# Kernel optimization log

Measured on AMD Instinct MI355X. Metric: run time of the kernel, lower is better.

## Reference

```python
import jax, jax.numpy as jnp
import numpy as np

MARGIN = 0.5
EPS = 1e-5
NOISE_RATE = 0.5


def setup_inputs() -> dict:
    key = jax.random.key(0)
    k1, k2, k3, k4, k5 = jax.random.split(key, 5)
    n, m, d, c = 1024, 65536, 512, 10000
    return {
        "inputs_col": jax.random.normal(k1, (n, d), dtype=jnp.float32),
        "inputs_row": jax.random.normal(k2, (m, d), dtype=jnp.float32),
        "center": jax.random.normal(k3, (c, d), dtype=jnp.float32),
        "targets_col": jax.random.randint(k4, (n,), 0, c, dtype=jnp.int64),
        "target_row": jax.random.randint(k5, (m,), 0, c, dtype=jnp.int64),
        "filled_mask": jnp.ones((c,), dtype=bool),
    }


def _prism_keep(features, targets, center, filled_mask, noise_rate):
    # no_grad in the original -> stop_gradient here
    f = jax.lax.stop_gradient(features)
    c = jax.lax.stop_gradient(center)
    # all_sim_exp[cls] / sum(all_sim_exp) is exactly softmax over class logits
    probs = jax.nn.softmax(f @ c.T, axis=-1)          # [n, num_classes]
    sel = jnp.take_along_axis(probs, targets[:, None], axis=1)[:, 0]  # [n]
    C = jnp.where(filled_mask[targets], sel, 1.0)      # not-in-memory -> 1
    n = C.shape[0]
    n_remove = int(noise_rate * n)                     # static
    to_remove = jnp.argsort(C)[:n_remove]
    # empty margin_window path: keep everything except to_remove
    keep = jnp.ones((n,), dtype=bool).at[to_remove].set(False)
    return keep


def reference(inputs_col, inputs_row, center, targets_col, target_row, filled_mask):
    n = inputs_col.shape[0]
    sim = inputs_col @ inputs_row.T                    # [n, m]
    pos_mask = targets_col[:, None] == target_row[None, :]
    neg_mask = (~pos_mask) & (sim > MARGIN)
    pos_mask = pos_mask & (sim < 1.0 - EPS)

    keep = _prism_keep(inputs_col, targets_col, center, filled_mask, NOISE_RATE)
    pos_mask = pos_mask & keep[:, None]
    neg_mask = neg_mask & keep[:, None]

    # sum over selected pairs without boolean-indexing (masked reductions)
    pos_loss = jnp.sum(jnp.where(pos_mask, 1.0 - sim, 0.0))
    neg_loss = jnp.sum(jnp.where(neg_mask, sim, 0.0))
    loss = (pos_loss + neg_loss) / n
    return loss, keep
```

## Files before the change

kernel.cpp:

```cpp
#include <hip/hip_runtime.h>


typedef int    v4i   __attribute__((ext_vector_type(4)));
typedef float  f32x4 __attribute__((ext_vector_type(4)));
typedef unsigned char u8;

#define N_COL  1024
#define M_ROW  65536
#define DDIM   512
#define NCLS   10000
#define NT     79
#define NREM   512

#define OFF_A8   0u
#define OFF_C8   524288u
#define OFF_PMS  39256064u
#define OFF_LT   39903232u
#define OFF_COMP 39907328u
#define OFF_TCC  39909376u
#define OFF_ACC  39911424u
#define OFF_CNT  39911432u

__device__ __forceinline__ void async16(const void* g, void* l) {
    __builtin_amdgcn_global_load_lds(
        (const __attribute__((address_space(1))) void*)g,
        (__attribute__((address_space(3))) void*)l, 16, 0, 0);
}

__device__ __forceinline__ unsigned pack4_fp8(float4 v) {
    int r = 0;
    r = __builtin_amdgcn_cvt_pk_fp8_f32(v.x, v.y, r, false);
    r = __builtin_amdgcn_cvt_pk_fp8_f32(v.z, v.w, r, true);
    return (unsigned)r;
}

__device__ __forceinline__ void gemm8_128(const u8* __restrict__ A,
                                          const u8* __restrict__ B,
                                          int m0, int n0,
                                          u8* As, u8* Bs, f32x4 (&acc)[4][4]) {
    const int tid = threadIdx.x, wid = tid >> 6, lane = tid & 63;
    const int wm = wid >> 1, wn = wid & 1;
    const int q = lane >> 4, lc = lane & 15;

    const u8* gA[4]; const u8* gB[4]; int voff[4];
#pragma unroll
    for (int s = 0; s < 4; ++s) {
        const int c  = wid * 256 + s * 64 + lane;
        const int r  = c >> 3;
        const int gs = (c & 7) ^ (r & 7);
        gA[s] = A + (size_t)(m0 + r) * DDIM + gs * 16;
        gB[s] = B + (size_t)(n0 + r) * DDIM + gs * 16;
        voff[s] = c * 16;
    }
#pragma unroll
    for (int i = 0; i < 4; ++i)
#pragma unroll
        for (int j = 0; j < 4; ++j) acc[i][j] = (f32x4){0.f, 0.f, 0.f, 0.f};

    for (int kt = 0; kt < 4; ++kt) {
        const int kb = kt * 128;
#pragma unroll
        for (int s = 0; s < 4; ++s) {
            async16(gA[s] + kb, As + voff[s]);
            async16(gB[s] + kb, Bs + voff[s]);
        }
        __syncthreads();
#pragma unroll
        for (int ks = 0; ks < 4; ++ks) {
            const int gg = ks * 2 + (q >> 1);
            const int bo = (q & 1) * 8;
            long long af[4], bv[4];
#pragma unroll
            for (int i = 0; i < 4; ++i) {
                const int rA = wm * 64 + i * 16 + lc;
                af[i] = *(const long long*)(As + (rA * 8 + (gg ^ (rA & 7))) * 16 + bo);
                const int rB = wn * 64 + i * 16 + lc;
                bv[i] = *(const long long*)(Bs + (rB * 8 + (gg ^ (rB & 7))) * 16 + bo);
            }
#pragma unroll
            for (int i = 0; i < 4; ++i)
#pragma unroll
                for (int j = 0; j < 4; ++j)
                    acc[i][j] = __builtin_amdgcn_mfma_f32_16x16x32_fp8_fp8(
                        af[i], bv[j], acc[i][j], 0, 0, 0);
        }
        __syncthreads();
    }
}

__global__ void k_prep(const float4* __restrict__ a4, const float4* __restrict__ c4,
                       const float* __restrict__ a32, const float* __restrict__ c32,
                       const int* __restrict__ tcol,
                       unsigned* __restrict__ A8w, uint2* __restrict__ C8w,
                       float* __restrict__ lt, double* __restrict__ accd,
                       unsigned* __restrict__ cnt) {
    const int b = blockIdx.x, tid = threadIdx.x;
    if (b == 0 && tid == 0) { *accd = 0.0; *cnt = 0u; }
    if (b < 256) {
        const int idx = b * 256 + tid;
        A8w[idx * 2]     = pack4_fp8(a4[idx * 2]);
        A8w[idx * 2 + 1] = pack4_fp8(a4[idx * 2 + 1]);
    } else if (b < 2784) {
        const int cidx = (b - 256) * 256 + tid;
        const int row  = cidx >> 6;
        uint2 o = make_uint2(0u, 0u);
        if (row < NCLS) {
            o.x = pack4_fp8(c4[cidx * 2]);
            o.y = pack4_fp8(c4[cidx * 2 + 1]);
        }
        C8w[cidx] = o;
    } else {
        const int w = (b - 2784) * 4 + (tid >> 6), lane = tid & 63;
        const int t = tcol[w];
        const float* ar = a32 + (size_t)w * DDIM;
        const float* cr = c32 + (size_t)t * DDIM;
        float s = 0.f;
#pragma unroll
        for (int k = 0; k < DDIM / 64; ++k) s += ar[lane + k * 64] * cr[lane + k * 64];
        for (int off = 32; off; off >>= 1) s += __shfl_down(s, off, 64);
        if (lane == 0) lt[w] = s;
    }
}

__global__ __launch_bounds__(256, 3) void k_mid(const u8* __restrict__ A8,
                                                const u8* __restrict__ C8,
                                                float2* __restrict__ pms) {
    const int b = blockIdx.x, tid = threadIdx.x;
    __shared__ __align__(16) u8 As[16384], Bs[16384];
    __shared__ float s_mm[128][2], s_ss[128][2];
    const int n_t = b >> 3, m0 = (b & 7) * 128, n0 = n_t * 128;
    f32x4 acc[4][4];
    gemm8_128(A8, C8, m0, n0, As, Bs, acc);

    const int wid = tid >> 6, lane = tid & 63;
    const int wm = wid >> 1, wn = wid & 1, q = lane >> 4, lc = lane & 15;
    const int cbase = n0 + wn * 64 + lc;
#pragma unroll
    for (int i = 0; i < 4; ++i) {
#pragma unroll
        for (int reg = 0; reg < 4; ++reg) {
            float mm = -INFINITY, ss = 0.f;
#pragma unroll
            for (int j = 0; j < 4; ++j)
                if (cbase + j * 16 < NCLS) mm = fmaxf(mm, acc[i][j][reg]);
#pragma unroll
            for (int j = 0; j < 4; ++j)
                if (cbase + j * 16 < NCLS) ss += __expf(acc[i][j][reg] - mm);
#pragma unroll
            for (int d2 = 1; d2 < 16; d2 <<= 1) {
                float mo = __shfl_xor(mm, d2, 16);
                float so = __shfl_xor(ss, d2, 16);
                float M = fmaxf(mm, mo), S = 0.f;
                if (ss > 0.f) S += ss * __expf(mm - M);
                if (so > 0.f) S += so * __expf(mo - M);
                mm = M; ss = S;
            }
            if (lc == 0) {
                const int row = i * 16 + q * 4 + reg;
                s_mm[wm * 64 + row][wn] = mm;
                s_ss[wm * 64 + row][wn] = ss;
            }
        }
    }
    __syncthreads();
    if (tid < 128) {
        float m1 = s_mm[tid][0], s1 = s_ss[tid][0];
        float m2 = s_mm[tid][1], s2 = s_ss[tid][1];
        float M = fmaxf(m1, m2), S = 0.f;
        if (s1 > 0.f) S += s1 * __expf(m1 - M);
        if (s2 > 0.f) S += s2 * __expf(m2 - M);
        pms[(size_t)n_t * N_COL + m0 + tid] = make_float2(M, S);
    }
}

__global__ __launch_bounds__(1024) void k_sel(const float2* __restrict__ pms,
                                              const float* __restrict__ lt,
                                              const int* __restrict__ tcol,
                                              int* __restrict__ comp,
                                              int* __restrict__ tcc,
                                              float* __restrict__ keep_out) {
    __shared__ float v[N_COL];
    const int i = threadIdx.x;
    float M = -INFINITY, S = 0.f;
    for (int t = 0; t < NT; ++t) {
        float2 p = pms[(size_t)t * N_COL + i];
        if (p.y > 0.f) {
            if (p.x > M) { S = S * __expf(M - p.x) + p.y; M = p.x; }
            else         { S += p.y * __expf(p.x - M); }
        }
    }
    const float x = lt[i] - (M + logf(S));
    v[i] = x;
    __syncthreads();
    int rank = 0;
    const float4* v4 = (const float4*)v;
#pragma unroll 8
    for (int j4 = 0; j4 < N_COL / 4; ++j4) {
        float4 w = v4[j4];
        const int j = j4 * 4;
        rank += (w.x < x) || (w.x == x && j     < i);
        rank += (w.y < x) || (w.y == x && j + 1 < i);
        rank += (w.z < x) || (w.z == x && j + 2 < i);
        rank += (w.w < x) || (w.w == x && j + 3 < i);
    }
    const bool keep = rank >= NREM;
    keep_out[i] = keep ? 1.0f : 0.0f;
    if (keep) { comp[rank - NREM] = i; tcc[rank - NREM] = tcol[i]; }
}

__global__ __launch_bounds__(512, 2) void k_loss(const u8* __restrict__ A8,
                                                 const float4* __restrict__ brow4,
                                                 const int* __restrict__ comp,
                                                 const int* __restrict__ tcc,
                                                 const int* __restrict__ trow,
                                                 double* __restrict__ accd,
                                                 unsigned* __restrict__ cnt,
                                                 float* __restrict__ out) {
    __shared__ __align__(16) u8 As[2][32768];
    __shared__ __align__(16) u8 Bs[2][8192];
    __shared__ int s_map[512], s_tc[512], s_tr[128];
    __shared__ float s_red[8];
    const int b = blockIdx.x, tid = threadIdx.x;
    const int n0 = b * 128;
    s_map[tid] = comp[tid];
    s_tc[tid]  = tcc[tid];
    if (tid < 128) s_tr[tid] = trow[n0 + tid];
    __syncthreads();

    const int wid = tid >> 6, lane = tid & 63;
    const int wm = wid >> 1, wn = wid & 1;
    const int q = lane >> 4, lc = lane & 15;

    const u8* gA[4]; int vA[4];
#pragma unroll
    for (int s = 0; s < 4; ++s) {
        const int cc = s * 512 + tid;
        const int r  = cc >> 2, gs = (cc & 3) ^ (r & 3);
        gA[s] = A8 + (size_t)s_map[r] * DDIM + gs * 16;
        vA[s] = cc * 16;
    }
    const int rB0 = tid >> 2, gB0 = tid & 3;
    const float4* gB = brow4 + (size_t)(n0 + rB0) * (DDIM / 4) + gB0 * 4;
    const int vB = (rB0 * 4 + (gB0 ^ (rB0 & 3))) * 16;

    f32x4 acc[8][4];
#pragma unroll
    for (int i = 0; i < 8; ++i)
#pragma unroll
        for (int j = 0; j < 4; ++j) acc[i][j] = (f32x4){0.f, 0.f, 0.f, 0.f};

    auto compute = [&](const u8* Asc, const u8* Bsc) {
#pragma unroll
        for (int ks = 0; ks < 2; ++ks) {
            const int gg = ks * 2 + (q >> 1);
            const int bo = (q & 1) * 8;
            long long af[8], bv[4];
#pragma unroll
            for (int i = 0; i < 8; ++i) {
                const int rA = wm * 128 + i * 16 + lc;
                af[i] = *(const long long*)(Asc + (rA * 4 + (gg ^ (rA & 3))) * 16 + bo);
            }
#pragma unroll
            for (int j = 0; j < 4; ++j) {
                const int rB = wn * 64 + j * 16 + lc;
                bv[j] = *(const long long*)(Bsc + (rB * 4 + (gg ^ (rB & 3))) * 16 + bo);
            }
#pragma unroll
            for (int i = 0; i < 8; ++i)
#pragma unroll
                for (int j = 0; j < 4; ++j)
                    acc[i][j] = __builtin_amdgcn_mfma_f32_16x16x32_fp8_fp8(
                        af[i], bv[j], acc[i][j], 0, 0, 0);
        }
    };

    {
#pragma unroll
        for (int s = 0; s < 4; ++s) async16(gA[s], As[0] + vA[s]);
        float4 f0 = gB[0], f1 = gB[1], f2 = gB[2], f3 = gB[3];
        uint4 pk;
        pk.x = pack4_fp8(f0); pk.y = pack4_fp8(f1);
        pk.z = pack4_fp8(f2); pk.w = pack4_fp8(f3);
        *(uint4*)(Bs[0] + vB) = pk;
        __syncthreads();
    }
    int cur = 0;
    for (int kt = 0; kt < 7; ++kt) {
        const int nxt = cur ^ 1;
        const int kb  = (kt + 1) * 64;
#pragma unroll
        for (int s = 0; s < 4; ++s) async16(gA[s] + kb, As[nxt] + vA[s]);
        const float4* gb = gB + (size_t)(kt + 1) * 16;
        float4 f0 = gb[0], f1 = gb[1], f2 = gb[2], f3 = gb[3];

        compute(As[cur], Bs[cur]);

        uint4 pk;
        pk.x = pack4_fp8(f0); pk.y = pack4_fp8(f1);
        pk.z = pack4_fp8(f2); pk.w = pack4_fp8(f3);
        *(uint4*)(Bs[nxt] + vB) = pk;
        __syncthreads();
        cur = nxt;
    }
    compute(As[cur], Bs[cur]);

    const float POSMAX = 1.0f - 1e-5f;
    float local = 0.f;
#pragma unroll
    for (int i = 0; i < 8; ++i) {
#pragma unroll
        for (int j = 0; j < 4; ++j) {
            const int tr = s_tr[wn * 64 + j * 16 + lc];
#pragma unroll
            for (int reg = 0; reg < 4; ++reg) {
                const int row = wm * 128 + i * 16 + q * 4 + reg;
                const float sim = acc[i][j][reg];
                if (s_tc[row] == tr) {
                    if (sim < POSMAX) local += 1.0f - sim;
                } else if (sim > 0.5f) {
                    local += sim;
                }
            }
        }
    }
    for (int off = 32; off; off >>= 1) local += __shfl_down(local, off, 64);
    if (lane == 0) s_red[wid] = local;
    __syncthreads();
    if (tid == 0) {
        float blk = 0.f;
#pragma unroll
        for (int w = 0; w < 8; ++w) blk += s_red[w];
        atomicAdd(accd, (double)blk);
        __threadfence();
        if (atomicAdd(cnt, 1u) == 511u) {
            double vfin = atomicAdd(accd, 0.0);
            out[0] = (float)(vfin / (double)N_COL);
        }
    }
}

extern "C" void kernel_launch(void* const* d_in, const int* in_sizes, int n_in,
                              void* d_out, int out_size, void* d_ws, size_t ws_size,
                              hipStream_t stream) {
    (void)in_sizes; (void)n_in; (void)out_size; (void)ws_size;
    const float* inputs_col  = (const float*)d_in[0];
    const float* inputs_row  = (const float*)d_in[1];
    const float* center      = (const float*)d_in[2];
    const int*   targets_col = (const int*)d_in[3];
    const int*   target_row  = (const int*)d_in[4];
    float* out = (float*)d_out;
    char*  ws  = (char*)d_ws;

    u8*       A8   = (u8*)(ws + OFF_A8);
    u8*       C8   = (u8*)(ws + OFF_C8);
    float2*   pms  = (float2*)(ws + OFF_PMS);
    float*    lt   = (float*) (ws + OFF_LT);
    int*      comp = (int*)   (ws + OFF_COMP);
    int*      tcc  = (int*)   (ws + OFF_TCC);
    double*   accd = (double*)(ws + OFF_ACC);
    unsigned* cnt  = (unsigned*)(ws + OFF_CNT);

    k_prep<<<3040, 256, 0, stream>>>((const float4*)inputs_col, (const float4*)center,
                                     inputs_col, center, targets_col,
                                     (unsigned*)A8, (uint2*)C8, lt, accd, cnt);
    k_mid<<<632, 256, 0, stream>>>(A8, C8, pms);
    k_sel<<<1, 1024, 0, stream>>>(pms, lt, targets_col, comp, tcc, out + 1);
    k_loss<<<512, 512, 0, stream>>>(A8, (const float4*)inputs_row,
                                    comp, tcc, target_row, accd, cnt, out);
}
```

Before: 332.4 us.

## Split selection kernel across blocks and change LDS swizzle in loss GEMM

The single-block selection kernel is split into a 16-block log-sum-exp kernel and a 16-block ranking kernel, so the 1024-row reduction and the O(n^2) rank computation spread over several compute units instead of one. This adds an extra launch and a global round-trip for the per-row log-probabilities. Separately, the LDS XOR swizzle in the fp8 loss GEMM now uses (row>>1)&3 instead of row&3, to cut bank conflicts on the 8-byte fragment reads.

```diff
diff --git a/kernel.cpp b/kernel.cpp
--- a/kernel.cpp
+++ b/kernel.cpp
@@ -18,8 +18,9 @@
 #define OFF_LT   39903232u
 #define OFF_COMP 39907328u
 #define OFF_TCC  39909376u
-#define OFF_ACC  39911424u
-#define OFF_CNT  39911432u
+#define OFF_LOGC 39911424u
+#define OFF_ACC  39915520u
+#define OFF_CNT  39915528u
 
 __device__ __forceinline__ void async16(const void* g, void* l) {
     __builtin_amdgcn_global_load_lds(
@@ -173,14 +174,10 @@
     }
 }
 
-__global__ __launch_bounds__(1024) void k_sel(const float2* __restrict__ pms,
-                                              const float* __restrict__ lt,
-                                              const int* __restrict__ tcol,
-                                              int* __restrict__ comp,
-                                              int* __restrict__ tcc,
-                                              float* __restrict__ keep_out) {
-    __shared__ float v[N_COL];
-    const int i = threadIdx.x;
+__global__ void k_lse(const float2* __restrict__ pms,
+                      const float* __restrict__ lt,
+                      float* __restrict__ logc) {
+    const int i = blockIdx.x * 64 + threadIdx.x;
     float M = -INFINITY, S = 0.f;
     for (int t = 0; t < NT; ++t) {
         float2 p = pms[(size_t)t * N_COL + i];
@@ -189,9 +186,23 @@
             else         { S += p.y * __expf(p.x - M); }
         }
     }
-    const float x = lt[i] - (M + logf(S));
-    v[i] = x;
+    logc[i] = lt[i] - (M + logf(S));
+}
+
+__global__ __launch_bounds__(64) void k_rank(const float* __restrict__ logc,
+                                             const int* __restrict__ tcol,
+                                             int* __restrict__ comp,
+                                             int* __restrict__ tcc,
+                                             float* __restrict__ keep_out) {
+    __shared__ float v[N_COL];
+    const int t = threadIdx.x, b = blockIdx.x;
+    const float4* g4 = (const float4*)logc;
+    float4* vs = (float4*)v;
+#pragma unroll
+    for (int s = 0; s < 4; ++s) vs[t + s * 64] = g4[t + s * 64];
     __syncthreads();
+    const int i = b * 64 + t;
+    const float x = v[i];
     int rank = 0;
     const float4* v4 = (const float4*)v;
 #pragma unroll 8
@@ -235,13 +246,14 @@
 #pragma unroll
     for (int s = 0; s < 4; ++s) {
         const int cc = s * 512 + tid;
-        const int r  = cc >> 2, gs = (cc & 3) ^ (r & 3);
-        gA[s] = A8 + (size_t)s_map[r] * DDIM + gs * 16;
+        const int r  = cc >> 2, gpos = cc & 3;
+        const int g  = gpos ^ ((r >> 1) & 3);
+        gA[s] = A8 + (size_t)s_map[r] * DDIM + g * 16;
         vA[s] = cc * 16;
     }
     const int rB0 = tid >> 2, gB0 = tid & 3;
     const float4* gB = brow4 + (size_t)(n0 + rB0) * (DDIM / 4) + gB0 * 4;
-    const int vB = (rB0 * 4 + (gB0 ^ (rB0 & 3))) * 16;
+    const int vB = (rB0 * 4 + (gB0 ^ ((rB0 >> 1) & 3))) * 16;
 
     f32x4 acc[8][4];
 #pragma unroll
@@ -258,12 +270,12 @@
 #pragma unroll
             for (int i = 0; i < 8; ++i) {
                 const int rA = wm * 128 + i * 16 + lc;
-                af[i] = *(const long long*)(Asc + (rA * 4 + (gg ^ (rA & 3))) * 16 + bo);
+                af[i] = *(const long long*)(Asc + (rA * 4 + (gg ^ ((rA >> 1) & 3))) * 16 + bo);
             }
 #pragma unroll
             for (int j = 0; j < 4; ++j) {
                 const int rB = wn * 64 + j * 16 + lc;
-                bv[j] = *(const long long*)(Bsc + (rB * 4 + (gg ^ (rB & 3))) * 16 + bo);
+                bv[j] = *(const long long*)(Bsc + (rB * 4 + (gg ^ ((rB >> 1) & 3))) * 16 + bo);
             }
 #pragma unroll
             for (int i = 0; i < 8; ++i)
@@ -357,6 +369,7 @@
     float*    lt   = (float*) (ws + OFF_LT);
     int*      comp = (int*)   (ws + OFF_COMP);
     int*      tcc  = (int*)   (ws + OFF_TCC);
+    float*    logc = (float*) (ws + OFF_LOGC);
     double*   accd = (double*)(ws + OFF_ACC);
     unsigned* cnt  = (unsigned*)(ws + OFF_CNT);
 
@@ -364,7 +377,8 @@
                                      inputs_col, center, targets_col,
                                      (unsigned*)A8, (uint2*)C8, lt, accd, cnt);
     k_mid<<<632, 256, 0, stream>>>(A8, C8, pms);
-    k_sel<<<1, 1024, 0, stream>>>(pms, lt, targets_col, comp, tcc, out + 1);
+    k_lse<<<16, 64, 0, stream>>>(pms, lt, logc);
+    k_rank<<<16, 64, 0, stream>>>(logc, targets_col, comp, tcc, out + 1);
     k_loss<<<512, 512, 0, stream>>>(A8, (const float4*)inputs_row,
                                     comp, tcc, target_row, accd, cnt, out);
 }
```

New measurement: 318.1 us. 1.05x faster.
